# Kernel optimization log

Measured on AMD Instinct MI355X. Metric: run time of the kernel, lower is better.

## Reference

```python
import jax, jax.numpy as jnp
import numpy as np

MAX_LR = 0.01  # max_learning_rate
NS_A, NS_B, NS_C = 3.4445, -4.7750, 2.0315  # muon Newton-Schulz quintic coefficients


def newtonschulz5(G, steps=5, eps=1e-7):
    # Orthogonalize the last two dims of G (batched over leading dims).
    transpose = G.shape[-2] > G.shape[-1]
    X = jnp.swapaxes(G, -2, -1) if transpose else G
    X = X / (jnp.linalg.norm(X, axis=(-2, -1), keepdims=True) + eps)
    for _ in range(steps):
        A = X @ jnp.swapaxes(X, -2, -1)
        Bm = NS_B * A + NS_C * (A @ A)
        X = NS_A * X + Bm @ X
    return jnp.swapaxes(X, -2, -1) if transpose else X


def setup_inputs() -> dict:
    key = jax.random.key(0)
    ks = jax.random.split(key, 9)
    B, N, D, H, DH = 4, 1024, 1024, 8, 64
    s = D ** -0.5  # scale fast-weight init for numerical sanity (math unchanged)
    return {
        'tokens': jax.random.normal(ks[0], (B, N, D), jnp.float32),
        'wq': jax.random.normal(ks[1], (H, D, DH), jnp.float32) * s,
        'wk': jax.random.normal(ks[2], (H, D, DH), jnp.float32) * s,
        'wv': jax.random.normal(ks[3], (H, D, DH), jnp.float32) * s,
        'wo': jax.random.normal(ks[4], (H, DH, D), jnp.float32) * s,
        'w_lr': jax.random.normal(ks[5], (D, 2), jnp.float32) * 0.02,      # to_learning_rate (no bias)
        'w_target': jax.random.normal(ks[6], (D, D), jnp.float32) * 0.02,  # to_target_values linear (no bias)
        'w_gates': jax.random.normal(ks[7], (D, H), jnp.float32) * 0.02,   # to_gates linear (no bias)
        'rms_w': jnp.ones((D,), jnp.float32),                              # RMSNorm weight
    }


def reference(tokens, wq, wk, wv, wo, w_lr, w_target, w_gates, rms_w):
    N = tokens.shape[1]
    scale = wq.shape[-1] ** -0.5
    eps = jnp.finfo(tokens.dtype).eps

    # RMSNorm
    t = tokens * jax.lax.rsqrt(jnp.mean(tokens * tokens, -1, keepdims=True) + eps) * rms_w

    # gates: b n h -> b h n 1
    gates = jnp.swapaxes(jax.nn.sigmoid(t @ w_gates), -2, -1)[..., None]

    # per-batch fast weights == shared params (past_mem=None), broadcast over b via einsum
    q = jnp.einsum('bnd,hde->bhne', t, wq)
    k = jnp.einsum('bnd,hde->bhne', t, wk)
    v = jnp.einsum('bnd,hde->bhne', t, wv)

    score = jnp.einsum('bhie,bhje->bhij', q, k) * scale
    causal_mask = jnp.triu(jnp.ones((N, N), bool), 1)
    score = jnp.where(causal_mask, -jnp.finfo(score.dtype).max, score)
    attn = jax.nn.softmax(score, axis=-1)
    out = jnp.einsum('bhij,bhje->bhie', attn, v) * gates
    pred_values = jnp.einsum('bhne,hed->bnd', out, wo)

    # target values: linear + LayerNorm (no affine) on shifted tokens
    tv = t[:, 1:] @ w_target
    tv = (tv - tv.mean(-1, keepdims=True)) * jax.lax.rsqrt(tv.var(-1, keepdims=True) + 1e-5)

    # drop last position everywhere
    ts = t[:, :-1]
    pv = pred_values[:, :-1]
    o = out[:, :, :-1]
    g = gates[:, :, :-1]
    a = attn[:, :, :-1, :-1]
    qs, ks_, vs = q[:, :, :-1], k[:, :, :-1], v[:, :, :-1]

    lrs = jax.nn.sigmoid(ts @ w_lr) * MAX_LR  # b (n-1) 2
    lr, mlr = lrs[..., 0], lrs[..., 1]

    # hand-derived backward through the attention fast-weight readout
    error = tv - pv
    dout = jnp.einsum('bnd,hed->bhne', error, wo)
    du = dout * g
    delta = jnp.sum(dout * o, -1, keepdims=True)
    dv = jnp.einsum('bhij,bhie->bhje', a, du)
    dattn = jnp.einsum('bhje,bhie->bhij', vs, du)
    dscore = scale * a * (dattn - delta)
    dq = jnp.einsum('bhje,bhij->bhie', ks_, dscore)
    dk = jnp.einsum('bhie,bhij->bhje', qs, dscore)

    t_qk = ts * lr[..., None]
    t_v = ts * mlr[..., None]
    o_wo = o * mlr[:, None, :, None]

    dwq = jnp.einsum('bhie,bid->bhde', dq, t_qk)
    dwk = jnp.einsum('bhje,bjd->bhde', dk, t_qk)
    dwv = jnp.einsum('bhje,bjd->bhde', dv, t_v)
    dwo = jnp.einsum('bnd,bhne->bhed', error, o_wo)

    dwv = newtonschulz5(dwv)  # muon orthogonalization
    dwo = newtonschulz5(dwo)

    return pred_values, dwq, dwk, dwv, dwo
```

## Files before the change

kernel.cpp:

```cpp
#include <hip/hip_runtime.h>
#include <hip/hip_bf16.h>
#include <math.h>

#define BB 4
#define NN 1024
#define DD 1024
#define HH 8
#define DH 64
#define NSR 1023

#define NS_Ac 3.4445f
#define NS_Bc (-4.775f)
#define NS_Cc 2.0315f

typedef short bf16x8 __attribute__((ext_vector_type(8)));
typedef float f32x4 __attribute__((ext_vector_type(4)));
#define MFMA16(a,b,c) __builtin_amdgcn_mfma_f32_16x16x32_bf16(a,b,c,0,0,0)

#define QS 72
#define TS 40
#define GS 40

static __device__ __forceinline__ float ldin(const void* p, size_t i, int f) {
  return f ? ((const float*)p)[i] : __bfloat162float(((const __hip_bfloat16*)p)[i]);
// ... 520 lines not shown
}

__global__ void k_lnsub(const float* __restrict__ tvbuf, float* __restrict__ predf,
                        short* __restrict__ err_bf) {
  int r = blockIdx.x; int b = r / 1023; int prow = r + b;
  const float* tvr = tvbuf + (size_t)r*1024;
  __shared__ float red[256];
  float s1 = 0.f, s2 = 0.f;
  float xv[4];
#pragma unroll
  for (int i = 0; i < 4; i++) {
    xv[i] = tvr[threadIdx.x + 256*i];
    s1 += xv[i]; s2 += xv[i]*xv[i];
  }
  red[threadIdx.x] = s1; __syncthreads();
  for (int s = 128; s > 0; s >>= 1){ if (threadIdx.x < s) red[threadIdx.x] += red[threadIdx.x+s]; __syncthreads(); }
  float mean = red[0] / 1024.f; __syncthreads();
  red[threadIdx.x] = s2; __syncthreads();
  for (int s = 128; s > 0; s >>= 1){ if (threadIdx.x < s) red[threadIdx.x] += red[threadIdx.x+s]; __syncthreads(); }
  float var = red[0]/1024.f - mean*mean;
  float rstd = rsqrtf(var + 1e-5f);
  float* er = predf + (size_t)prow*1024;
#pragma unroll
  for (int i = 0; i < 4; i++) {
    int d = threadIdx.x + 256*i;
    float e = (xv[i]-mean)*rstd - er[d];
    er[d] = e;
    err_bf[(size_t)prow*1024 + d] = f2bs(e);
  }
}

__global__ __launch_bounds__(256) void k_t16(const short* __restrict__ qv, const short* __restrict__ du,
                                             short* __restrict__ kbT, short* __restrict__ duT,
                                             short* __restrict__ qbT,
                                             const float* __restrict__ o, const float* __restrict__ gates,
                                             float* __restrict__ delta) {
  int bx = blockIdx.x; int tid = threadIdx.x;
  if (bx >= 1536) {
    int r = bx - 1536; int b = r / 1023; int n = r % 1023;
    int w = tid >> 6, lane = tid & 63;
    size_t base = ((size_t)b*1024 + n)*512;
    float p1 = bs2f(du[base + tid])       * o[base + tid];
    float p2 = bs2f(du[base + tid + 256]) * o[base + tid + 256];
    for (int s = 32; s > 0; s >>= 1) { p1 += __shfl_xor(p1, s, 64); p2 += __shfl_xor(p2, s, 64); }
    if (lane == 0) {
      size_t i1 = ((size_t)b*8 + w)*1024 + n;
      size_t i2 = ((size_t)b*8 + w + 4)*1024 + n;
      delta[i1] = p1 / gates[i1];
      delta[i2] = p2 / gates[i2];
    }
    return;
  }
  int z = bx >> 4;
  int r0 = (bx & 15)*64;
  const short* sb; short* db; int sld, nvalid;
  if (z < 32) {
    sb = qv + (size_t)(32 + z)*65536; sld = 64; nvalid = 1024;
    db = kbT + (size_t)z*65536;
  } else if (z < 64) {
    int zz = z - 32;
    sb = du + (size_t)(zz >> 3)*524288 + (size_t)(zz & 7)*64;
    sld = 512; nvalid = 1023;
    db = duT + (size_t)zz*65536;
  } else {
    int zz = z - 64;
    sb = qv + (size_t)zz*65536; sld = 64; nvalid = 1024;
    db = qbT + (size_t)zz*65536;
  }
  __shared__ float T[64][65];
  int sr = tid >> 3, sc = (tid & 7)*8;
  for (int rr = sr; rr < 64; rr += 32) {
    int n = r0 + rr;
    bf16x8 v = (n < nvalid) ? *(const bf16x8*)&sb[(size_t)n*sld + sc] : bz8();
#pragma unroll
    for (int j = 0; j < 8; j++) T[rr][sc+j] = bs2f(v[j]);
  }
  __syncthreads();
  int dc = tid >> 2, seg = tid & 3;
  bf16x8 o1, o2;
#pragma unroll
  for (int j = 0; j < 8; j++) { o1[j] = f2bs(T[seg*16+j][dc]); o2[j] = f2bs(T[seg*16+8+j][dc]); }
  *(bf16x8*)&db[(size_t)dc*1024 + r0 + seg*16]     = o1;
  *(bf16x8*)&db[(size_t)dc*1024 + r0 + seg*16 + 8] = o2;
}

__global__ __launch_bounds__(256) void k_bwd(
    const short* __restrict__ qb, const short* __restrict__ kb, const short* __restrict__ vb,
    const short* __restrict__ du_bf, const short* __restrict__ qbT, const short* __restrict__ duT,
    const short* __restrict__ kbT,
    const float* __restrict__ mrow, const float* __restrict__ lrow, const float* __restrict__ delta,
    float* __restrict__ dv, float* __restrict__ dk, float* __restrict__ dq)
{
  __shared__ __align__(16) short smem[24320];
  int tid = threadIdx.x;
  int lane = tid & 63, w = tid >> 6;
  int l15 = lane & 15, quad = lane >> 4;
  int sr = tid >> 3, sc = (tid & 7) * 8;
  int sr2 = tid >> 2, sc2 = (tid & 3) * 8;
  int rsw = (l15 >> 2) & 3;

  if (blockIdx.x < 512) {
    int pp = blockIdx.x >> 8;
    int xx = (blockIdx.x >> 5) & 7;
    int bh = blockIdx.x & 31;
    int jt = pp ? (15 - xx) : xx;
    int j0 = jt*64;
    int b = bh >> 3, h = bh & 7;
    short* Ks   = smem;
    short* Vs   = Ks + 4608;
    short* Qs   = Vs + 4608;
    short* DUs  = Qs + 2304;
    short* QsT  = DUs + 2304;
    short* DUsT = QsT + 2560;
    short* PsT  = DUsT + 2560;
    short* DsT  = PsT + 2560;
    float* mvs  = (float*)(DsT + 2560);
    float* lvs  = mvs + 32;
    float* dls  = lvs + 32;
    for (int rr = sr; rr < 64; rr += 32) {
      *(bf16x8*)&Ks[rr*QS + sc] = *(const bf16x8*)&kb[((size_t)bh*1024 + j0 + rr)*64 + sc];
      *(bf16x8*)&Vs[rr*QS + sc] = *(const bf16x8*)&vb[((size_t)bh*1024 + j0 + rr)*64 + sc];
    }
    f32x4 dva[4] = {fz4(),fz4(),fz4(),fz4()};
    f32x4 dka[4] = {fz4(),fz4(),fz4(),fz4()};
    int iters = 32 - 2*jt;
    int gi0 = j0 + sr;
    bf16x8 rq   = *(const bf16x8*)&qb[((size_t)bh*1024 + gi0)*64 + sc];
    bf16x8 rdu  = (gi0 < NSR) ? *(const bf16x8*)&du_bf[((size_t)b*1024 + gi0)*512 + h*64 + sc] : bz8();
    bf16x8 rqT  = *(const bf16x8*)&qbT[((size_t)bh*64 + sr2)*1024 + j0 + sc2];
    bf16x8 rduT = *(const bf16x8*)&duT[((size_t)bh*64 + sr2)*1024 + j0 + sc2];
    float rm = 0.f, rl = 1.f, rd = 0.f;
    if (tid < 32) {
      int gi2 = j0 + tid;
      rm = mrow[(size_t)bh*1024 + gi2];
      rl = lrow[(size_t)bh*1024 + gi2];
      rd = (gi2 < NSR) ? delta[(size_t)bh*1024 + gi2] : 0.f;
    }
    for (int ic = 0; ic < iters; ic++) {
      int i0c = j0 + ic*32;
      __syncthreads();
      *(bf16x8*)&Qs[sr*QS + sc]    = rq;
      *(bf16x8*)&DUs[sr*QS + sc]   = rdu;
      *(bf16x8*)&QsT[sr2*TS + sc2]  = rqT;
      *(bf16x8*)&DUsT[sr2*TS + sc2] = rduT;
      if (tid < 32) { mvs[tid] = rm; lvs[tid] = 1.f/rl; dls[tid] = rd; }
      __syncthreads();
      if (ic + 1 < iters) {
        int i1 = i0c + 32;
        int g1 = i1 + sr;
        rq   = *(const bf16x8*)&qb[((size_t)bh*1024 + g1)*64 + sc];
        rdu  = (g1 < NSR) ? *(const bf16x8*)&du_bf[((size_t)b*1024 + g1)*512 + h*64 + sc] : bz8();
        rqT  = *(const bf16x8*)&qbT[((size_t)bh*64 + sr2)*1024 + i1 + sc2];
        rduT = *(const bf16x8*)&duT[((size_t)bh*64 + sr2)*1024 + i1 + sc2];
        if (tid < 32) {
          int gi2 = i1 + tid;
          rm = mrow[(size_t)bh*1024 + gi2];
          rl = lrow[(size_t)bh*1024 + gi2];
          rd = (gi2 < NSR) ? delta[(size_t)bh*1024 + gi2] : 0.f;
        }
      }
      f32x4 st[2] = {fz4(),fz4()};
      f32x4 dt[2] = {fz4(),fz4()};
#pragma unroll
      for (int kc = 0; kc < 64; kc += 32) {
        bf16x8 ak = *(const bf16x8*)&Ks[(w*16 + l15)*QS + kc + quad*8];
        bf16x8 av = *(const bf16x8*)&Vs[(w*16 + l15)*QS + kc + quad*8];
#pragma unroll
        for (int ni = 0; ni < 2; ni++) {
          bf16x8 bq = *(const bf16x8*)&Qs[(ni*16 + l15)*QS + kc + quad*8];
          bf16x8 bd = *(const bf16x8*)&DUs[(ni*16 + l15)*QS + kc + quad*8];
          st[ni] = MFMA16(ak, bq, st[ni]);
          dt[ni] = MFMA16(av, bd, dt[ni]);
        }
      }
#pragma unroll
      for (int ni = 0; ni < 2; ni++)
#pragma unroll
        for (int r = 0; r < 4; r++) {
          int gj = j0 + w*16 + quad*4 + r;
          int il = ni*16 + l15;
          int gi = i0c + il;
          float p = 0.f, dsc = 0.f;
          if (gi >= gj && gi < NSR && gj < NSR) {
            p = __expf(st[ni][r]*0.125f - mvs[il]) * lvs[il];
            dsc = 0.125f*p*(dt[ni][r] - dls[il]);
          }
          int rowp = w*16 + quad*4 + r;
          int pc = ((((ni << 1) | (l15 >> 3)) ^ quad) << 3) | (l15 & 7);
          PsT[rowp*TS + pc] = f2bs(p);
          DsT[rowp*TS + pc] = f2bs(dsc);
        }
      int rc = (quad ^ rsw) << 3;
      bf16x8 ap = *(const bf16x8*)&PsT[(w*16 + l15)*TS + rc];
      bf16x8 ad = *(const bf16x8*)&DsT[(w*16 + l15)*TS + rc];
#pragma unroll
      for (int es = 0; es < 4; es++) {
        bf16x8 bdu = *(const bf16x8*)&DUsT[(es*16 + l15)*TS + quad*8];
        bf16x8 bqt = *(const bf16x8*)&QsT[(es*16 + l15)*TS + quad*8];
        dva[es] = MFMA16(ap, bdu, dva[es]);
        dka[es] = MFMA16(ad, bqt, dka[es]);
      }
    }
#pragma unroll
    for (int r = 0; r < 4; r++) {
      int gj = j0 + w*16 + quad*4 + r;
#pragma unroll
      for (int es = 0; es < 4; es++) {
        dv[((size_t)bh*1024 + gj)*64 + es*16 + l15] = dva[es][r];
        dk[((size_t)bh*1024 + gj)*64 + es*16 + l15] = dka[es][r];
      }
    }
  } else {
    int bid = blockIdx.x - 512;
    int pp = bid >> 8;
    int xx = (bid >> 5) & 7;
    int bh = bid & 31;
    int it = pp ? xx : (15 - xx);
    int i0 = it*64;
    int b = bh >> 3, h = bh & 7;
    short* Qs  = smem;
    short* DUs = Qs + 4608;
    short* Ks  = DUs + 4608;
    short* Vs  = Ks + 2304;
    short* KsT = Vs + 2304;
    short* DsN = KsT + 2560;
    for (int rr = sr; rr < 64; rr += 32) {
      int gi = i0 + rr;
      *(bf16x8*)&Qs[rr*QS + sc] = *(const bf16x8*)&qb[((size_t)bh*1024 + gi)*64 + sc];
      bf16x8 duv = (gi < NSR) ? *(const bf16x8*)&du_bf[((size_t)b*1024 + gi)*512 + h*64 + sc] : bz8();
      *(bf16x8*)&DUs[rr*QS + sc] = duv;
    }
    float m4[4], li4[4], dl4[4];
#pragma unroll
    for (int r = 0; r < 4; r++) {
      int gi = i0 + w*16 + quad*4 + r;
      m4[r]  = mrow[(size_t)bh*1024 + gi];
      li4[r] = 1.f / lrow[(size_t)bh*1024 + gi];
      dl4[r] = (gi < NSR) ? delta[(size_t)bh*1024 + gi] : 0.f;
    }
    f32x4 dqa[4] = {fz4(),fz4(),fz4(),fz4()};
    int jiters = 2*it + 2;
    bf16x8 rk  = *(const bf16x8*)&kb[((size_t)bh*1024 + sr)*64 + sc];
    bf16x8 rv  = *(const bf16x8*)&vb[((size_t)bh*1024 + sr)*64 + sc];
    bf16x8 rkT = *(const bf16x8*)&kbT[((size_t)bh*64 + sr2)*1024 + sc2];
    for (int jc = 0; jc < jiters; jc++) {
      int j0 = jc*32;
      __syncthreads();
      *(bf16x8*)&Ks[sr*QS + sc]    = rk;
      *(bf16x8*)&Vs[sr*QS + sc]    = rv;
      *(bf16x8*)&KsT[sr2*TS + sc2] = rkT;
      __syncthreads();
      if (jc + 1 < jiters) {
        int j1 = j0 + 32;
        rk  = *(const bf16x8*)&kb[((size_t)bh*1024 + j1 + sr)*64 + sc];
        rv  = *(const bf16x8*)&vb[((size_t)bh*1024 + j1 + sr)*64 + sc];
        rkT = *(const bf16x8*)&kbT[((size_t)bh*64 + sr2)*1024 + j1 + sc2];
      }
      f32x4 st[2] = {fz4(),fz4()};
      f32x4 dt[2] = {fz4(),fz4()};
#pragma unroll
      for (int kc = 0; kc < 64; kc += 32) {
        bf16x8 aq = *(const bf16x8*)&Qs[(w*16 + l15)*QS + kc + quad*8];
        bf16x8 adu = *(const bf16x8*)&DUs[(w*16 + l15)*QS + kc + quad*8];
#pragma unroll
        for (int ni = 0; ni < 2; ni++) {
          bf16x8 bk = *(const bf16x8*)&Ks[(ni*16 + l15)*QS + kc + quad*8];
          bf16x8 bv = *(const bf16x8*)&Vs[(ni*16 + l15)*QS + kc + quad*8];
          st[ni] = MFMA16(aq, bk, st[ni]);
          dt[ni] = MFMA16(adu, bv, dt[ni]);
        }
      }
#pragma unroll
      for (int ni = 0; ni < 2; ni++)
#pragma unroll
        for (int r = 0; r < 4; r++) {
          int gi = i0 + w*16 + quad*4 + r;
          int gj = j0 + ni*16 + l15;
          float dsc = 0.f;
          if (gi >= gj && gi < NSR && gj < NSR) {
            float p = __expf(st[ni][r]*0.125f - m4[r]) * li4[r];
            dsc = 0.125f*p*(dt[ni][r] - dl4[r]);
          }
          int rowp = w*16 + quad*4 + r;
          int pc = ((((ni << 1) | (l15 >> 3)) ^ quad) << 3) | (l15 & 7);
          DsN[rowp*TS + pc] = f2bs(dsc);
        }
      bf16x8 ads = *(const bf16x8*)&DsN[(w*16 + l15)*TS + ((quad ^ rsw) << 3)];
#pragma unroll
      for (int es = 0; es < 4; es++) {
        bf16x8 bkt = *(const bf16x8*)&KsT[(es*16 + l15)*TS + quad*8];
        dqa[es] = MFMA16(ads, bkt, dqa[es]);
      }
    }
#pragma unroll
    for (int r = 0; r < 4; r++) {
      int gi = i0 + w*16 + quad*4 + r;
#pragma unroll
      for (int es = 0; es < 4; es++)
        dq[((size_t)bh*1024 + gi)*64 + es*16 + l15] = dqa[es][r];
    }
  }
}

__global__ __launch_bounds__(256) void k_ns_all(const float* __restrict__ Xsrc, void* __restrict__ d_outv,
                                                size_t off_dwv, size_t off_dwo, const int* __restrict__ flag) {
  int m = blockIdx.x;
  const float* Xm = Xsrc + (size_t)m*DH*DD;
  const int f = *flag;
  __shared__ __align__(16) short nsm[46080];
  __shared__ float redz[4];
  short* Mhi  = nsm;
  short* Mlo  = nsm + 4608;
  short* MThi = nsm + 2*4608;
  short* MTlo = nsm + 3*4608;
  short* A0hi = nsm + 4*4608;
  short* A0lo = nsm + 5*4608;
  short* Shi  = nsm + 6*4608;
  short* Slo  = nsm + 7*4608;
  short* Aihi = nsm + 8*4608;
  short* Ailo = nsm + 9*4608;
  short* XGhi = Shi;
  short* XGlo = Slo;
  short* XThi = Aihi;
  short* XTlo = Ailo;
  int tid = threadIdx.x;
  int lane = tid & 63, w = tid >> 6;
  int l15 = lane & 15, quad = lane >> 4;
  int srow = tid >> 2, scol = (tid & 3) * 8;
  f32x4 accA[4] = {fz4(),fz4(),fz4(),fz4()};
  float ss = 0.f;
  float4 c1 = *(const float4*)&Xm[(size_t)srow*1024 + scol];
  float4 c2 = *(const float4*)&Xm[(size_t)srow*1024 + scol + 4];
  for (int kb = 0; kb < 1024; kb += 32) {
    float xv[8] = {c1.x,c1.y,c1.z,c1.w,c2.x,c2.y,c2.z,c2.w};
    bf16x8 hi, lo;
#pragma unroll
    for (int j = 0; j < 8; j++) {
      short h = f2bs(xv[j]);
      hi[j] = h; lo[j] = f2bs(xv[j] - bs2f(h));
      ss += xv[j]*xv[j];
    }
    __syncthreads();
    *(bf16x8*)&XGhi[srow*GS + scol] = hi;
    *(bf16x8*)&XGlo[srow*GS + scol] = lo;
    __syncthreads();
    if (kb + 32 < 1024) {
      c1 = *(const float4*)&Xm[(size_t)srow*1024 + kb + 32 + scol];
      c2 = *(const float4*)&Xm[(size_t)srow*1024 + kb + 32 + scol + 4];
    }
    bf16x8 ah = *(const bf16x8*)&XGhi[(w*16 + l15)*GS + quad*8];
    bf16x8 al = *(const bf16x8*)&XGlo[(w*16 + l15)*GS + quad*8];
#pragma unroll
    for (int es = 0; es < 4; es++) {
      bf16x8 bh = *(const bf16x8*)&XGhi[(es*16 + l15)*GS + quad*8];
      bf16x8 bl = *(const bf16x8*)&XGlo[(es*16 + l15)*GS + quad*8];
      accA[es] = MFMA16(ah, bh, accA[es]);
      accA[es] = MFMA16(ah, bl, accA[es]);
      accA[es] = MFMA16(al, bh, accA[es]);
    }
  }
  for (int s = 32; s > 0; s >>= 1) ss += __shfl_xor(ss, s, 64);
  __syncthreads();
  if (lane == 0) redz[w] = ss;
  __syncthreads();
  float tot = redz[0]+redz[1]+redz[2]+redz[3];
  float r_ = 1.f / (sqrtf(tot) + 1e-7f);
  float r2 = r_ * r_;
  __syncthreads();
#pragma unroll
  for (int es = 0; es < 4; es++)
#pragma unroll
    for (int rr = 0; rr < 4; rr++) {
      int row = w*16 + quad*4 + rr, col = es*16 + l15;
      float v = accA[es][rr] * r2;
      short h = f2bs(v);
      A0hi[row*QS + col] = h;
      A0lo[row*QS + col] = f2bs(v - bs2f(h));
      short ih = (row == col) ? (short)0x3F80 : (short)0;
      Mhi[row*QS + col] = ih;  Mlo[row*QS + col] = 0;
      MThi[row*QS + col] = ih; MTlo[row*QS + col] = 0;
    }
  __syncthreads();
  for (int itn = 0; itn < 5; itn++) {
    f32x4 s4[4] = {fz4(),fz4(),fz4(),fz4()};
    mm64(Mhi, Mlo, A0hi, A0lo, s4, w, l15, quad);
    st_hl(Shi, Slo, s4, w, l15, quad);
    __syncthreads();
    f32x4 ai4[4] = {fz4(),fz4(),fz4(),fz4()};
    mm64(Shi, Slo, Mhi, Mlo, ai4, w, l15, quad);
    st_hl(Aihi, Ailo, ai4, w, l15, quad);
    __syncthreads();
    f32x4 a24[4] = {fz4(),fz4(),fz4(),fz4()};
    mm64(Aihi, Ailo, Aihi, Ailo, a24, w, l15, quad);
    f32x4 b4[4];
#pragma unroll
    for (int es = 0; es < 4; es++) b4[es] = NS_Bc*ai4[es] + NS_Cc*a24[es];
    st_hl(Shi, Slo, b4, w, l15, quad);
    __syncthreads();
    f32x4 m4[4] = {fz4(),fz4(),fz4(),fz4()};
    mm64(Shi, Slo, MThi, MTlo, m4, w, l15, quad);
#pragma unroll
    for (int es = 0; es < 4; es++)
#pragma unroll
      for (int rr = 0; rr < 4; rr++) {
        int row = w*16 + quad*4 + rr, col = es*16 + l15;
        float mold = bs2f(Mhi[row*QS + col]) + bs2f(Mlo[row*QS + col]);
        m4[es][rr] = NS_Ac*mold + m4[es][rr];
      }
    __syncthreads();
#pragma unroll
    for (int es = 0; es < 4; es++)
#pragma unroll
      for (int rr = 0; rr < 4; rr++) {
        int row = w*16 + quad*4 + rr, col = es*16 + l15;
        float x = m4[es][rr];
        short h = f2bs(x);
        short lo = f2bs(x - bs2f(h));
        Mhi[row*QS + col] = h;  Mlo[row*QS + col] = lo;
        MThi[col*QS + row] = h; MTlo[col*QS + row] = lo;
      }
    __syncthreads();
  }
  float* Sf = (float*)Shi;
  float4 d1 = *(const float4*)&Xm[(size_t)srow*1024 + scol];
  float4 d2 = *(const float4*)&Xm[(size_t)srow*1024 + scol + 4];
  float4 d3 = *(const float4*)&Xm[(size_t)srow*1024 + scol + 32];
  float4 d4 = *(const float4*)&Xm[(size_t)srow*1024 + scol + 36];
  for (int c0 = 0; c0 < 1024; c0 += 64) {
    __syncthreads();
    {
      float xv0[8] = {d1.x,d1.y,d1.z,d1.w,d2.x,d2.y,d2.z,d2.w};
      float xv1[8] = {d3.x,d3.y,d3.z,d3.w,d4.x,d4.y,d4.z,d4.w};
#pragma unroll
      for (int j = 0; j < 8; j++) {
        int n0 = scol + j;
        short h0 = f2bs(xv0[j]);
        XThi[n0*QS + srow] = h0;
        XTlo[n0*QS + srow] = f2bs(xv0[j] - bs2f(h0));
        int n1 = scol + 32 + j;
        short h1 = f2bs(xv1[j]);
        XThi[n1*QS + srow] = h1;
        XTlo[n1*QS + srow] = f2bs(xv1[j] - bs2f(h1));
      }
    }
    __syncthreads();
    if (c0 + 64 < 1024) {
      d1 = *(const float4*)&Xm[(size_t)srow*1024 + c0 + 64 + scol];
      d2 = *(const float4*)&Xm[(size_t)srow*1024 + c0 + 64 + scol + 4];
      d3 = *(const float4*)&Xm[(size_t)srow*1024 + c0 + 64 + scol + 32];
      d4 = *(const float4*)&Xm[(size_t)srow*1024 + c0 + 64 + scol + 36];
    }
    f32x4 u4[4] = {fz4(),fz4(),fz4(),fz4()};
    mm64(Mhi, Mlo, XThi, XTlo, u4, w, l15, quad);
    if (m >= 32) {
#pragma unroll
      for (int es = 0; es < 4; es++)
#pragma unroll
        for (int rr = 0; rr < 4; rr++) {
          int row = w*16 + quad*4 + rr, col = c0 + es*16 + l15;
          stout(d_outv, off_dwo + (size_t)(m-32)*65536 + (size_t)row*1024 + col, r_*u4[es][rr], f);
        }
    } else {
#pragma unroll
      for (int es = 0; es < 4; es++)
#pragma unroll
        for (int rr = 0; rr < 4; rr++) {
          int row = w*16 + quad*4 + rr, col = es*16 + l15;
          Sf[col*65 + row] = r_*u4[es][rr];
        }
      __syncthreads();
      int dl = tid >> 2, e0 = (tid & 3)*16;
      size_t ob = off_dwv + (size_t)m*65536 + (size_t)(c0 + dl)*64 + e0;
#pragma unroll
      for (int j = 0; j < 16; j++)
        stout(d_outv, ob + j, Sf[dl*65 + e0 + j], f);
    }
  }
}

extern "C" void kernel_launch(void* const* d_in, const int* in_sizes, int n_in,
                              void* d_out, int out_size, void* d_ws, size_t ws_size,
                              hipStream_t stream) {
  const void* tokens   = d_in[0];
  const void* wq       = d_in[1];
  const void* wk       = d_in[2];
  const void* wv       = d_in[3];
  const void* wo       = d_in[4];
  const void* w_lr     = d_in[5];
  const void* w_target = d_in[6];
  const void* w_gates  = d_in[7];
  const void* rms_w    = d_in[8];

  const size_t off_dwq  = 4194304;
  const size_t off_dwk  = 6291456;
  const size_t off_dwv  = 8388608;
  const size_t off_dwo  = 10485760;

  float* ws = (float*)d_ws;
  float* t_    = ws;
  float* tvbuf = ws;
  short* errT  = (short*)ws;
  short* oT    = (short*)(ws + 2097152);
  short* t_bf  = (short*)(ws + 4194304);
  short* err_bf= (short*)(ws + 4194304);
  short* tT    = (short*)(ws + 6291456);
  short* qb    = (short*)(ws + 8388608);
  short* kbuf  = qb + 2097152;
  short* vbuf  = qb + 4194304;
  short* dqT   = (short*)(ws + 8388608);
  short* dkT   = dqT + 2097152;
  short* dvT   = dqT + 4194304;
  float* o_    = ws + 11534336;
  short* o_bf  = (short*)(ws + 13631488);
  short* du_bf = (short*)(ws + 13631488);
  float* predf = ws + 14680064;
  float* Xns   = ws + 14680064;
  short* BqkvT = (short*)(ws + 18874368);
  short* wtT   = (short*)(ws + 19660800);
  short* woT2  = (short*)(ws + 20185088);
  short* wo_bf = (short*)(ws + 20447232);
  float* gw    = ws + 20709376;
  float* lrw   = ws + 20717568;
  float* rms_f = ws + 20719616;
  float* dv_   = ws + 18874368;
  float* dk_   = ws + 20971520;
  float* dq_   = ws + 23068672;
  float* gates_= ws + 25165824;
  float* mrow_ = ws + 25198592;
  float* lrow_ = ws + 25231360;
  float* delta_= ws + 25264128;
  float* lr_   = ws + 25296896;
  float* mlr_  = ws + 25300992;
  int*   flag_ = (int*)(ws + 25305088);
  short* vbT = (short*)(ws + 3145728);
  short* duT = (short*)(ws + 3145728);
  short* kbT = (short*)(ws + 4194304);
  short* qbT = (short*)ws;

  hipLaunchKernelGGL(k_prep, dim3(1324), dim3(256), 0, stream, wq, wk, wv, w_target, wo, w_lr, w_gates, rms_w,
                     BqkvT, wtT, woT2, wo_bf, lrw, gw, rms_f, flag_);
  hipLaunchKernelGGL(k_rmsnorm, dim3(BB*NN), dim3(256), 0, stream, tokens, rms_f, gw, lrw,
                     t_, t_bf, gates_, lr_, mlr_, flag_);
  hipLaunchKernelGGL(k_transp, dim3(64,16,1), dim3(256), 0, stream, t_, (size_t)0, 1024, tT, (size_t)0, 4096, (const float*)nullptr, 0, 4096);

  hipLaunchKernelGGL(k_gemm2, dim3(32,12), dim3(256), 0, stream, t_bf, BqkvT, 1024, 1024, 1024, 4096, 0, 0,
                     (float*)nullptr, qb, (void*)nullptr, vbT, (const float*)nullptr, flag_);
  hipLaunchKernelGGL(k_attn_fwd, dim3(512), dim3(256), 0, stream, qb, kbuf, vbT, gates_, o_, o_bf, mrow_, lrow_);
  hipLaunchKernelGGL(k_gemm2, dim3(32,8), dim3(256), 0, stream, o_bf, woT2, 512, 512, 512, 4096, 0, 1,
                     predf, (short*)nullptr, d_out, (short*)nullptr, (const float*)nullptr, flag_);
  hipLaunchKernelGGL(k_gemm2, dim3(32,8), dim3(256), 0, stream, t_bf, wtT, 1024, 1024, 1024, 4092, 1, 2,
                     tvbuf, (short*)nullptr, (void*)nullptr, (short*)nullptr, (const float*)nullptr, flag_);
  hipLaunchKernelGGL(k_lnsub, dim3(BB*NSR), dim3(256), 0, stream, tvbuf, predf, err_bf);
  hipLaunchKernelGGL(k_gemm2, dim3(32,4), dim3(256), 0, stream, err_bf, wo_bf, 1024, 1024, 1024, 4092, 2, 3,
                     (float*)nullptr, du_bf, (void*)nullptr, (short*)nullptr, gates_, flag_);
  hipLaunchKernelGGL(k_t16, dim3(1536 + BB*NSR), dim3(256), 0, stream, (const short*)qb, (const short*)du_bf,
                     kbT, duT, qbT, o_, gates_, delta_);
  hipLaunchKernelGGL(k_bwd, dim3(1024), dim3(256), 0, stream, qb, kbuf, vbuf, du_bf, qbT, duT, kbT,
                     mrow_, lrow_, delta_, dv_, dk_, dq_);
  hipLaunchKernelGGL(k_transp5, dim3(3072), dim3(256), 0, stream, dq_, dk_, dv_, predf, o_,
                     dqT, dkT, dvT, errT, oT, lr_, mlr_);
  hipLaunchKernelGGL(k_gemm_bf, dim3(16,1,64), dim3(256), 0, stream, tT, dqT, 4096, 1024, 1024, 1024, 0, 4,
                     (size_t)0,(size_t)1024,(size_t)65536,(size_t)0, (float*)nullptr, (short*)nullptr, d_out, off_dwq,
                     (const float*)nullptr, flag_, (const short*)nullptr, (const short*)dkT, (size_t)0, off_dwk, 1024);
  hipLaunchKernelGGL(k_gemm_bf, dim3(1,16,64), dim3(256), 0, stream, dvT, tT, 1024, 4096, 1024, 64, 0, 5,
                     (size_t)65536,(size_t)0,(size_t)0,(size_t)1024, Xns, (short*)nullptr, (void*)nullptr, (size_t)0,
                     (const float*)nullptr, flag_, (const short*)oT, (const short*)errT, (size_t)1048576, (size_t)0, 1024);
  hipLaunchKernelGGL(k_ns_all, dim3(64), dim3(256), 0, stream, Xns, d_out, off_dwv, off_dwo, flag_);
  (void)in_sizes; (void)n_in; (void)out_size; (void)ws_size;
}
```

Measured before the change: 503.1 us.

## Split Newton-Schulz kernel into Gram, iterate, and apply stages for more parallelism

The single 64-block Newton-Schulz kernel is split into three kernels. A 64x4-block kernel computes partial Gram matrices and partial squared norms over K-chunks. A 64-block kernel reduces those partials and runs the small 64x64 iterations. A 64x4-block kernel then applies the resulting matrix to column slices of X. This lets the large Gram and apply phases fill more compute units on the GPU, which otherwise sat mostly idle with 64 blocks. The cost is two extra launches and some workspace traffic for the partials and the M5 matrix.

After: 471.3 us. -6.3%, faster.

```diff
diff --git a/kernel.cpp b/kernel.cpp
--- a/kernel.cpp
+++ b/kernel.cpp
@@ -846,13 +846,67 @@
   }
 }
 
-__global__ __launch_bounds__(256) void k_ns_all(const float* __restrict__ Xsrc, void* __restrict__ d_outv,
-                                                size_t off_dwv, size_t off_dwo, const int* __restrict__ flag) {
+__global__ __launch_bounds__(256) void k_ns_g(const float* __restrict__ Xsrc,
+                                              float* __restrict__ Gpart, float* __restrict__ sspart) {
+  int m = blockIdx.x, s = blockIdx.y;
+  const float* Xm = Xsrc + (size_t)m*DH*DD;
+  __shared__ __align__(16) short XGhi[64*GS], XGlo[64*GS];
+  __shared__ float redz[4];
+  int tid = threadIdx.x;
+  int lane = tid & 63, w = tid >> 6;
+  int l15 = lane & 15, quad = lane >> 4;
+  int srow = tid >> 2, scol = (tid & 3)*8;
+  int k0 = s*256;
+  f32x4 accA[4] = {fz4(),fz4(),fz4(),fz4()};
+  float ss = 0.f;
+  float4 c1 = *(const float4*)&Xm[(size_t)srow*1024 + k0 + scol];
+  float4 c2 = *(const float4*)&Xm[(size_t)srow*1024 + k0 + scol + 4];
+  for (int kb = 0; kb < 256; kb += 32) {
+    float xv[8] = {c1.x,c1.y,c1.z,c1.w,c2.x,c2.y,c2.z,c2.w};
+    bf16x8 hi, lo;
+#pragma unroll
+    for (int j = 0; j < 8; j++) {
+      short h = f2bs(xv[j]);
+      hi[j] = h; lo[j] = f2bs(xv[j] - bs2f(h));
+      ss += xv[j]*xv[j];
+    }
+    __syncthreads();
+    *(bf16x8*)&XGhi[srow*GS + scol] = hi;
+    *(bf16x8*)&XGlo[srow*GS + scol] = lo;
+    __syncthreads();
+    if (kb + 32 < 256) {
+      c1 = *(const float4*)&Xm[(size_t)srow*1024 + k0 + kb + 32 + scol];
+      c2 = *(const float4*)&Xm[(size_t)srow*1024 + k0 + kb + 32 + scol + 4];
+    }
+    bf16x8 ah = *(const bf16x8*)&XGhi[(w*16 + l15)*GS + quad*8];
+    bf16x8 al = *(const bf16x8*)&XGlo[(w*16 + l15)*GS + quad*8];
+#pragma unroll
+    for (int es = 0; es < 4; es++) {
+      bf16x8 bh = *(const bf16x8*)&XGhi[(es*16 + l15)*GS + quad*8];
+      bf16x8 bl = *(const bf16x8*)&XGlo[(es*16 + l15)*GS + quad*8];
+      accA[es] = MFMA16(ah, bh, accA[es]);
+      accA[es] = MFMA16(ah, bl, accA[es]);
+      accA[es] = MFMA16(al, bh, accA[es]);
+    }
+  }
+  for (int st = 32; st > 0; st >>= 1) ss += __shfl_xor(ss, st, 64);
+  if (lane == 0) redz[w] = ss;
+  __syncthreads();
+  if (tid == 0) sspart[m*4 + s] = redz[0]+redz[1]+redz[2]+redz[3];
+  float* Gp = Gpart + (size_t)(m*4 + s)*4096;
+#pragma unroll
+  for (int es = 0; es < 4; es++)
+#pragma unroll
+    for (int rr = 0; rr < 4; rr++) {
+      int row = w*16 + quad*4 + rr, col = es*16 + l15;
+      Gp[row*64 + col] = accA[es][rr];
+    }
+}
+
+__global__ __launch_bounds__(256) void k_ns_iter(const float* __restrict__ Gpart, const float* __restrict__ sspart,
+                                                 float* __restrict__ M5, float* __restrict__ rbuf) {
   int m = blockIdx.x;
-  const float* Xm = Xsrc + (size_t)m*DH*DD;
-  const int f = *flag;
   __shared__ __align__(16) short nsm[46080];
-  __shared__ float redz[4];
   short* Mhi  = nsm;
   short* Mlo  = nsm + 4608;
   short* MThi = nsm + 2*4608;
@@ -863,60 +917,20 @@
   short* Slo  = nsm + 7*4608;
   short* Aihi = nsm + 8*4608;
   short* Ailo = nsm + 9*4608;
-  short* XGhi = Shi;
-  short* XGlo = Slo;
-  short* XThi = Aihi;
-  short* XTlo = Ailo;
   int tid = threadIdx.x;
   int lane = tid & 63, w = tid >> 6;
   int l15 = lane & 15, quad = lane >> 4;
-  int srow = tid >> 2, scol = (tid & 3) * 8;
-  f32x4 accA[4] = {fz4(),fz4(),fz4(),fz4()};
-  float ss = 0.f;
-  float4 c1 = *(const float4*)&Xm[(size_t)srow*1024 + scol];
-  float4 c2 = *(const float4*)&Xm[(size_t)srow*1024 + scol + 4];
-  for (int kb = 0; kb < 1024; kb += 32) {
-    float xv[8] = {c1.x,c1.y,c1.z,c1.w,c2.x,c2.y,c2.z,c2.w};
-    bf16x8 hi, lo;
-#pragma unroll
-    for (int j = 0; j < 8; j++) {
-      short h = f2bs(xv[j]);
-      hi[j] = h; lo[j] = f2bs(xv[j] - bs2f(h));
-      ss += xv[j]*xv[j];
-    }
-    __syncthreads();
-    *(bf16x8*)&XGhi[srow*GS + scol] = hi;
-    *(bf16x8*)&XGlo[srow*GS + scol] = lo;
-    __syncthreads();
-    if (kb + 32 < 1024) {
-      c1 = *(const float4*)&Xm[(size_t)srow*1024 + kb + 32 + scol];
-      c2 = *(const float4*)&Xm[(size_t)srow*1024 + kb + 32 + scol + 4];
-    }
-    bf16x8 ah = *(const bf16x8*)&XGhi[(w*16 + l15)*GS + quad*8];
-    bf16x8 al = *(const bf16x8*)&XGlo[(w*16 + l15)*GS + quad*8];
-#pragma unroll
-    for (int es = 0; es < 4; es++) {
-      bf16x8 bh = *(const bf16x8*)&XGhi[(es*16 + l15)*GS + quad*8];
-      bf16x8 bl = *(const bf16x8*)&XGlo[(es*16 + l15)*GS + quad*8];
-      accA[es] = MFMA16(ah, bh, accA[es]);
-      accA[es] = MFMA16(ah, bl, accA[es]);
-      accA[es] = MFMA16(al, bh, accA[es]);
-    }
-  }
-  for (int s = 32; s > 0; s >>= 1) ss += __shfl_xor(ss, s, 64);
-  __syncthreads();
-  if (lane == 0) redz[w] = ss;
-  __syncthreads();
-  float tot = redz[0]+redz[1]+redz[2]+redz[3];
+  float tot = sspart[m*4] + sspart[m*4+1] + sspart[m*4+2] + sspart[m*4+3];
   float r_ = 1.f / (sqrtf(tot) + 1e-7f);
   float r2 = r_ * r_;
-  __syncthreads();
+  const float* Gp = Gpart + (size_t)(m*4)*4096;
 #pragma unroll
   for (int es = 0; es < 4; es++)
 #pragma unroll
     for (int rr = 0; rr < 4; rr++) {
       int row = w*16 + quad*4 + rr, col = es*16 + l15;
-      float v = accA[es][rr] * r2;
+      int idx = row*64 + col;
+      float v = (Gp[idx] + Gp[4096 + idx] + Gp[8192 + idx] + Gp[12288 + idx]) * r2;
       short h = f2bs(v);
       A0hi[row*QS + col] = h;
       A0lo[row*QS + col] = f2bs(v - bs2f(h));
@@ -965,12 +979,43 @@
       }
     __syncthreads();
   }
-  float* Sf = (float*)Shi;
-  float4 d1 = *(const float4*)&Xm[(size_t)srow*1024 + scol];
-  float4 d2 = *(const float4*)&Xm[(size_t)srow*1024 + scol + 4];
-  float4 d3 = *(const float4*)&Xm[(size_t)srow*1024 + scol + 32];
-  float4 d4 = *(const float4*)&Xm[(size_t)srow*1024 + scol + 36];
-  for (int c0 = 0; c0 < 1024; c0 += 64) {
+#pragma unroll
+  for (int es = 0; es < 4; es++)
+#pragma unroll
+    for (int rr = 0; rr < 4; rr++) {
+      int row = w*16 + quad*4 + rr, col = es*16 + l15;
+      M5[(size_t)m*4096 + row*64 + col] = bs2f(Mhi[row*QS + col]) + bs2f(Mlo[row*QS + col]);
+    }
+  if (tid == 0) rbuf[m] = r_;
+}
+
+__global__ __launch_bounds__(256) void k_ns_apply(const float* __restrict__ Xsrc, const float* __restrict__ M5,
+                                                  const float* __restrict__ rbuf, void* __restrict__ d_outv,
+                                                  size_t off_dwv, size_t off_dwo, const int* __restrict__ flag) {
+  int m = blockIdx.x, cs = blockIdx.y;
+  const float* Xm = Xsrc + (size_t)m*DH*DD;
+  const int f = *flag;
+  float r_ = rbuf[m];
+  __shared__ __align__(16) short Mhi[4608], Mlo[4608], XThi[4608], XTlo[4608];
+  __shared__ float Sf[64*65];
+  int tid = threadIdx.x;
+  int lane = tid & 63, w = tid >> 6;
+  int l15 = lane & 15, quad = lane >> 4;
+  int srow = tid >> 2, scol = (tid & 3)*8;
+  for (int i = tid; i < 4096; i += 256) {
+    float v = M5[(size_t)m*4096 + i];
+    int rowi = i >> 6, coli = i & 63;
+    short h = f2bs(v);
+    Mhi[rowi*QS + coli] = h;
+    Mlo[rowi*QS + coli] = f2bs(v - bs2f(h));
+  }
+  int cbase = cs*256;
+  float4 d1 = *(const float4*)&Xm[(size_t)srow*1024 + cbase + scol];
+  float4 d2 = *(const float4*)&Xm[(size_t)srow*1024 + cbase + scol + 4];
+  float4 d3 = *(const float4*)&Xm[(size_t)srow*1024 + cbase + scol + 32];
+  float4 d4 = *(const float4*)&Xm[(size_t)srow*1024 + cbase + scol + 36];
+  for (int cc = 0; cc < 256; cc += 64) {
+    int c0 = cbase + cc;
     __syncthreads();
     {
       float xv0[8] = {d1.x,d1.y,d1.z,d1.w,d2.x,d2.y,d2.z,d2.w};
@@ -988,7 +1033,7 @@
       }
     }
     __syncthreads();
-    if (c0 + 64 < 1024) {
+    if (cc + 64 < 256) {
       d1 = *(const float4*)&Xm[(size_t)srow*1024 + c0 + 64 + scol];
       d2 = *(const float4*)&Xm[(size_t)srow*1024 + c0 + 64 + scol + 4];
       d3 = *(const float4*)&Xm[(size_t)srow*1024 + c0 + 64 + scol + 32];
@@ -1080,6 +1125,10 @@
   short* duT = (short*)(ws + 3145728);
   short* kbT = (short*)(ws + 4194304);
   short* qbT = (short*)ws;
+  float* Gpart  = ws + 18874368;
+  float* M5b    = ws + 19922944;
+  float* rbuf   = ws + 20185088;
+  float* sspart = ws + 20185152;
 
   hipLaunchKernelGGL(k_prep, dim3(1324), dim3(256), 0, stream, wq, wk, wv, w_target, wo, w_lr, w_gates, rms_w,
                      BqkvT, wtT, woT2, wo_bf, lrw, gw, rms_f, flag_);
@@ -1109,6 +1158,8 @@
   hipLaunchKernelGGL(k_gemm_bf, dim3(1,16,64), dim3(256), 0, stream, dvT, tT, 1024, 4096, 1024, 64, 0, 5,
                      (size_t)65536,(size_t)0,(size_t)0,(size_t)1024, Xns, (short*)nullptr, (void*)nullptr, (size_t)0,
                      (const float*)nullptr, flag_, (const short*)oT, (const short*)errT, (size_t)1048576, (size_t)0, 1024);
-  hipLaunchKernelGGL(k_ns_all, dim3(64), dim3(256), 0, stream, Xns, d_out, off_dwv, off_dwo, flag_);
+  hipLaunchKernelGGL(k_ns_g,     dim3(64,4), dim3(256), 0, stream, Xns, Gpart, sspart);
+  hipLaunchKernelGGL(k_ns_iter,  dim3(64),   dim3(256), 0, stream, Gpart, sspart, M5b, rbuf);
+  hipLaunchKernelGGL(k_ns_apply, dim3(64,4), dim3(256), 0, stream, Xns, M5b, rbuf, d_out, off_dwv, off_dwo, flag_);
   (void)in_sizes; (void)n_in; (void)out_size; (void)ws_size;
 }
```
